# Optimization experiments

Measured on AMD Instinct MI355X. Metric: run time of the kernel, lower is better.

The kernel has to match this reference:

```python
import jax, jax.numpy as jnp
import numpy as np

B, L, D = 8, 3072, 256
E = 4            # num_experts
K = 2            # num_experts_per_tok
H = 4 * D        # expert mlp hidden
HS = 4 * D * 1   # shared expert hidden (n_shared_experts=1)


def setup_inputs() -> dict:
    key = jax.random.key(0)
    ks = jax.random.split(key, 16)
    s = lambda *sh: 1.0 / np.sqrt(sh[0])
    return {
        "context_c": jax.random.normal(ks[0], (B, L, D), jnp.float32),
        "time_cond": jax.random.normal(ks[1], (B, D), jnp.float32),
        "gate_w": jax.random.normal(ks[2], (3 * D, E), jnp.float32) * s(3 * D),
        "gate_b": jnp.zeros((E,), jnp.float32),
        "tmod_w": jax.random.normal(ks[3], (D, 2 * E), jnp.float32) * 0.02,
        "tmod_b": jnp.zeros((2 * E,), jnp.float32),
        "ew1": jax.random.normal(ks[4], (E, D, H), jnp.float32) * s(D),
        "eb1": jnp.zeros((E, H), jnp.float32),
        "ew2": jax.random.normal(ks[5], (E, H, D), jnp.float32) * s(H),
        "eb2": jnp.zeros((E, D), jnp.float32),
        "sw1": jax.random.normal(ks[6], (D, HS), jnp.float32) * s(D),
        "sb1": jnp.zeros((HS,), jnp.float32),
        "sw2": jax.random.normal(ks[7], (HS, D), jnp.float32) * s(HS),
        "sb2": jnp.zeros((D,), jnp.float32),
    }


def reference(context_c, time_cond, gate_w, gate_b, tmod_w, tmod_b,
              ew1, eb1, ew2, eb2, sw1, sb1, sw2, sb2):
    x = context_c
    Bc, Lc, Dc = x.shape
    Lh = Lw = Lc // 3
    Lp = Lc - Lh - Lw

    # modality aggregates for gating
    head, wrist, prop = x[:, :Lh], x[:, Lh:Lh + Lw], x[:, Lh + Lw:]
    full_agg = x.mean(axis=1)
    hp_agg = (head.sum(axis=1) + prop.sum(axis=1)) / (Lh + Lp)   # mean of cat(head, proprio)
    wp_agg = (wrist.sum(axis=1) + prop.sum(axis=1)) / (Lw + Lp)  # mean of cat(wrist, proprio)
    gate_in = jnp.concatenate([full_agg, hp_agg, wp_agg], axis=-1)  # (B, 3D)

    gate_logits = gate_in @ gate_w + gate_b  # (B, E)
    # time-conditioned modulation: SiLU -> Linear -> chunk(scale, shift)
    mod = jax.nn.silu(time_cond) @ tmod_w + tmod_b
    scale, shift = jnp.split(mod, 2, axis=-1)
    gate_logits = gate_logits * (1.0 + scale) + shift

    gate_scores = jax.nn.softmax(gate_logits, axis=-1)
    topk_w, topk_i = jax.lax.top_k(gate_scores, K)
    topk_w = topk_w / (topk_w.sum(axis=-1, keepdims=True) + 1e-8)

    # dense per-expert token-wise MLP (equivalent to the gather: MLPs act per-token)
    h = jax.nn.gelu(jnp.einsum('bld,edh->belh', x, ew1) + eb1[None, :, None, :], approximate=True)
    y = jnp.einsum('belh,ehd->beld', h, ew2) + eb2[None, :, None, :]  # (B, E, L, D)

    # modality masks: expert 0 & >=3 -> all tokens; 1 -> head+proprio; 2 -> wrist+proprio
    pos = jnp.arange(Lc)
    is_head = pos < Lh
    is_wrist = (pos >= Lh) & (pos < Lh + Lw)
    is_prop = pos >= Lh + Lw
    mask = jnp.ones((E, Lc), x.dtype)
    mask = mask.at[1].set((is_head | is_prop).astype(x.dtype))
    mask = mask.at[2].set((is_wrist | is_prop).astype(x.dtype))

    # combine weights per (batch, expert) from top-k
    w_be = (jax.nn.one_hot(topk_i, E, dtype=x.dtype) * topk_w[..., None]).sum(axis=1)  # (B, E)
    out = jnp.einsum('be,beld,el->bld', w_be, y, mask)

    # shared expert
    out = out + (jax.nn.gelu(x @ sw1 + sb1, approximate=True) @ sw2 + sb2)
    return out


if __name__ == '__main__':
    o = reference(**setup_inputs())
    print(o.shape, o.dtype)
```

## Files before the change

kernel.cpp:

```cpp
#include <hip/hip_runtime.h>
#include <stdint.h>

#define Ddim 256
#define Hdim 1024
#define LSEQ 3072

typedef __bf16 bf16x8 __attribute__((ext_vector_type(8)));
typedef unsigned short u16x8 __attribute__((ext_vector_type(8)));
typedef float f32x4 __attribute__((ext_vector_type(4)));

#define MFMA(a, b, c) __builtin_amdgcn_mfma_f32_16x16x32_bf16( \
    __builtin_bit_cast(bf16x8, (a)), __builtin_bit_cast(bf16x8, (b)), (c), 0, 0, 0)

__device__ __forceinline__ unsigned short f2bf(float f) {
  unsigned int u = __float_as_uint(f);
  u = u + 0x7FFFu + ((u >> 16) & 1u);
  return (unsigned short)(u >> 16);
}

__device__ __forceinline__ float gelu_t(float x) {
  float t = 0.7978845608028654f * (x + 0.044715f * x * x * x);
  float e = __expf(2.0f * t);
  float th = 1.0f - 2.0f / (e + 1.0f);
  return 0.5f * x * (1.0f + th);
}

__device__ __forceinline__ int gate_list(const float* __restrict__ wbe, int b, int seg,
                                         int* widx, float* wsc) {
  float wv0 = wbe[b * 4 + 0], wv1 = wbe[b * 4 + 1];
  float wv2 = wbe[b * 4 + 2], wv3 = wbe[b * 4 + 3];
  int nm = 0;
  widx[nm] = 4; wsc[nm] = 1.0f; ++nm;
  if (wv0 > 0.0f) { widx[nm] = 0; wsc[nm] = wv0; ++nm; }
  if (wv1 > 0.0f && seg != 1) { widx[nm] = 1; wsc[nm] = wv1; ++nm; }
  if (wv2 > 0.0f && seg != 0) { widx[nm] = 2; wsc[nm] = wv2; ++nm; }
  if (wv3 > 0.0f && nm < 3) { widx[nm] = 3; wsc[nm] = wv3; ++nm; }
  return nm;
}

__device__ __forceinline__ void glds16(const unsigned short* g, unsigned short* l) {
  __builtin_amdgcn_global_load_lds(
      (const __attribute__((address_space(1))) unsigned int*)g,
      (__attribute__((address_space(3))) unsigned int*)l, 16, 0, 0);
}


__global__ void zero_seg(float* p) {
  p[blockIdx.x * 256 + threadIdx.x] = 0.0f;
}

__global__ void seg_reduce(const float* __restrict__ x, float* __restrict__ seg) {
  int lb = blockIdx.x, b = blockIdx.y, tid = threadIdx.x;
  const float* xg = x + ((size_t)b * LSEQ + (size_t)lb * 128) * Ddim + tid;
  float s = 0.0f;
  #pragma unroll 8
  for (int r = 0; r < 128; ++r) s += xg[(size_t)r * Ddim];
  int sg = lb >> 3;
  atomicAdd(&seg[(b * 3 + sg) * Ddim + tid], s);
}

__global__ void gate_kernel(const float* __restrict__ seg, const float* __restrict__ tc,
                            const float* __restrict__ gw, const float* __restrict__ gb,
                            const float* __restrict__ tw, const float* __restrict__ tb,
                            float* __restrict__ wbe) {
  int b = threadIdx.x >> 6, lane = threadIdx.x & 63;
  const float* sb_ = seg + b * 3 * 256;
  float pl[4] = {0.f, 0.f, 0.f, 0.f};
  for (int i = lane; i < 768; i += 64) {
    int d = i & 255, rg = i >> 8;
    float Sh = sb_[d], Sw = sb_[256 + d], Sp = sb_[512 + d];
    float val = (rg == 0) ? (Sh + Sw + Sp) * (1.0f / 3072.0f)
              : (rg == 1) ? (Sh + Sp) * (1.0f / 2048.0f)
                          : (Sw + Sp) * (1.0f / 2048.0f);
    #pragma unroll
    for (int e = 0; e < 4; ++e) pl[e] += val * gw[i * 4 + e];
  }
  float pm[8] = {0.f, 0.f, 0.f, 0.f, 0.f, 0.f, 0.f, 0.f};
  for (int d = lane; d < 256; d += 64) {
    float t = tc[b * 256 + d];
    float s = t / (1.0f + __expf(-t));
    #pragma unroll
    for (int j = 0; j < 8; ++j) pm[j] += s * tw[d * 8 + j];
  }
  #pragma unroll
  for (int off = 32; off > 0; off >>= 1) {
    #pragma unroll
    for (int e = 0; e < 4; ++e) pl[e] += __shfl_down(pl[e], off);
    #pragma unroll
    for (int j = 0; j < 8; ++j) pm[j] += __shfl_down(pm[j], off);
  }
  if (lane == 0) {
    #pragma unroll
    for (int j = 0; j < 8; ++j) pm[j] += tb[j];
    float lg[4], sc[4];
    #pragma unroll
    for (int e = 0; e < 4; ++e) lg[e] = (pl[e] + gb[e]) * (1.0f + pm[e]) + pm[4 + e];
    float mx = fmaxf(fmaxf(lg[0], lg[1]), fmaxf(lg[2], lg[3]));
    float s = 0.0f;
    #pragma unroll
    for (int e = 0; e < 4; ++e) { sc[e] = __expf(lg[e] - mx); s += sc[e]; }
    #pragma unroll
    for (int e = 0; e < 4; ++e) sc[e] /= s;
    int i1 = 0;
    #pragma unroll
    for (int e = 1; e < 4; ++e) if (sc[e] > sc[i1]) i1 = e;
    int i2 = (i1 == 0) ? 1 : 0;
    #pragma unroll
    for (int e = 0; e < 4; ++e) if (e != i1 && sc[e] > sc[i2]) i2 = e;
    float den = sc[i1] + sc[i2] + 1e-8f;
    #pragma unroll
    for (int e = 0; e < 4; ++e)
      wbe[b * 4 + e] = (e == i1) ? sc[i1] / den : ((e == i2) ? sc[i2] / den : 0.0f);
  }
}


__global__ void prep_w1f_v2(const float* __restrict__ ew1, const float* __restrict__ sw1,
                            unsigned short* __restrict__ wch) {
  int hc = blockIdx.x, id = blockIdx.y;
  const float* src = (id < 4) ? (ew1 + (size_t)id * Ddim * Hdim) : sw1;
  __shared__ float tile[256 * 33];
  int tid = threadIdx.x;
  int h0 = hc * 32;
  #pragma unroll
  for (int p = 0; p < 8; ++p) {
    int row = p * 32 + (tid >> 3);
    int c = (tid & 7) * 4;
    float4 v = *(const float4*)&src[(size_t)row * Hdim + h0 + c];
    tile[row * 33 + c] = v.x; tile[row * 33 + c + 1] = v.y;
    tile[row * 33 + c + 2] = v.z; tile[row * 33 + c + 3] = v.w;
  }
  __syncthreads();
  unsigned short* dst = wch + ((size_t)(id * 32 + hc)) * 16384;
  int lane = tid & 63, lr = lane & 15, lg = lane >> 4;
  #pragma unroll
  for (int p = 0; p < 4; ++p) {
    int f = tid + p * 256;
    int hg = (f >> 6) & 1, k = f >> 7;
    u16x8 r;
    #pragma unroll
    for (int j = 0; j < 8; ++j) r[j] = f2bf(tile[(k * 32 + lg * 8 + j) * 33 + hg * 16 + lr]);
    *(u16x8*)&dst[(size_t)f * 8] = r;
  }
}

__global__ void prep_w2f_v2(const float* __restrict__ ew2, const float* __restrict__ sw2,
                            unsigned short* __restrict__ wch) {
  int hc = blockIdx.x, id = blockIdx.y;
  const float* src = (id < 4) ? (ew2 + (size_t)id * Hdim * Ddim) : sw2;
  __shared__ float tile[32 * 264];
  int tid = threadIdx.x;
  int h0 = hc * 32;
  #pragma unroll
  for (int p = 0; p < 8; ++p) {
    int hh = p * 4 + (tid >> 6);
    int c = (tid & 63) * 4;
    float4 v = *(const float4*)&src[(size_t)(h0 + hh) * Ddim + c];
    int ci = c + (c >> 5);
    tile[hh * 264 + ci] = v.x; tile[hh * 264 + ci + 1] = v.y;
    tile[hh * 264 + ci + 2] = v.z; tile[hh * 264 + ci + 3] = v.w;
  }
  __syncthreads();
  unsigned short* dst = wch + ((size_t)(id * 32 + hc)) * 16384 + 8192;
  int lane = tid & 63, lr = lane & 15, lg = lane >> 4;
  #pragma unroll
  for (int p = 0; p < 4; ++p) {
    int f = tid + p * 256;
    int dg = f >> 6;
    u16x8 r;
    #pragma unroll
    for (int j = 0; j < 8; ++j) {
      int c = dg * 16 + lr;
      r[j] = f2bf(tile[(lg * 8 + j) * 264 + c + (c >> 5)]);
    }
    *(u16x8*)&dst[(size_t)f * 8] = r;
  }
}

__global__ __launch_bounds__(256, 2) void moe_main(
    const float* __restrict__ x, const unsigned short* __restrict__ wch,
    const float* __restrict__ eb1, const float* __restrict__ sb1,
    const float* __restrict__ eb2, const float* __restrict__ sb2,
    const float* __restrict__ wbe, float* __restrict__ out) {
  __shared__ __align__(16) unsigned short lds[2 * 16384 + 64 * 40];
  unsigned short* hid = lds + 32768;

  const int i = blockIdx.x;
  const int b = i & 7, t = i >> 3;
  const int tid = threadIdx.x;
  const int wave = tid >> 6, lane = tid & 63;
  const int lr = lane & 15, lg = lane >> 4;
  const int wm = wave >> 1, wn = wave & 1;
  const int seg = t >> 4;

  int widx[3]; float wsc[3];
  const int nm = gate_list(wbe, b, seg, widx, wsc);
  const int total = nm * 32;

  u16x8 xf[8][2];
  const float* xb = x + ((size_t)(b * LSEQ + t * 64 + wm * 32 + lr)) * Ddim;
  #pragma unroll
  for (int k = 0; k < 8; ++k) {
    #pragma unroll
    for (int mf = 0; mf < 2; ++mf) {
      const float* p = xb + (size_t)(mf * 16) * Ddim + k * 32 + lg * 8;
      float4 v0 = *(const float4*)p;
      float4 v1 = *(const float4*)(p + 4);
      u16x8 r;
      r[0] = f2bf(v0.x); r[1] = f2bf(v0.y); r[2] = f2bf(v0.z); r[3] = f2bf(v0.w);
      r[4] = f2bf(v1.x); r[5] = f2bf(v1.y); r[6] = f2bf(v1.z); r[7] = f2bf(v1.w);
      xf[k][mf] = r;
    }
  }

  f32x4 oacc[4][4];
  const f32x4 fz = {0.f, 0.f, 0.f, 0.f};
  #pragma unroll
  for (int mf = 0; mf < 4; ++mf)
    #pragma unroll
    for (int nf = 0; nf < 4; ++nf) oacc[mf][nf] = fz;

  {
    const unsigned short* src = wch + (size_t)(widx[0] * 32) * 16384 + tid * 8;
    unsigned short* l = lds + tid * 8;
    #pragma unroll
    for (int q = 0; q < 8; ++q) glds16(src + q * 2048, l + q * 2048);
  }
  __syncthreads();

  for (int j = 0; j < total; ++j) {
    unsigned short* cur = lds + (j & 1) * 16384;
    unsigned short* nxt = lds + ((j & 1) ^ 1) * 16384;

    if (j + 1 < total) {
      int m2 = (j + 1) >> 5, hc2 = (j + 1) & 31;
      const unsigned short* src = wch + (size_t)(widx[m2] * 32 + hc2) * 16384 + tid * 8;
      unsigned short* l = nxt + tid * 8;
      #pragma unroll
      for (int q = 0; q < 8; ++q) glds16(src + q * 2048, l + q * 2048);
    }

    const int m = j >> 5, hc = j & 31;
    const float* b1g = (widx[m] < 4) ? (eb1 + widx[m] * Hdim) : sb1;
    const float wscale = wsc[m];

    f32x4 a1[2];
    a1[0] = fz; a1[1] = fz;
    #pragma unroll
    for (int k = 0; k < 8; ++k) {
      u16x8 bf = *(const u16x8*)&cur[((k * 2 + wn) * 64 + lane) * 8];
      a1[0] = MFMA(xf[k][0], bf, a1[0]);
      a1[1] = MFMA(xf[k][1], bf, a1[1]);
    }
    float b1v = b1g[hc * 32 + wn * 16 + lr];
    #pragma unroll
    for (int mr = 0; mr < 2; ++mr)
      #pragma unroll
      for (int r = 0; r < 4; ++r)
        hid[(wm * 32 + mr * 16 + lg * 4 + r) * 40 + wn * 16 + lr] =
            f2bf(gelu_t(a1[mr][r] + b1v) * wscale);
    __syncthreads();

    u16x8 ha[4], wb[4];
    #pragma unroll
    for (int mf = 0; mf < 4; ++mf)
      ha[mf] = *(const u16x8*)&hid[(mf * 16 + lr) * 40 + lg * 8];
    #pragma unroll
    for (int nf = 0; nf < 4; ++nf)
      wb[nf] = *(const u16x8*)&cur[8192 + ((wave * 4 + nf) * 64 + lane) * 8];
    #pragma unroll
    for (int mf = 0; mf < 4; ++mf)
      #pragma unroll
      for (int nf = 0; nf < 4; ++nf)
        oacc[mf][nf] = MFMA(ha[mf], wb[nf], oacc[mf][nf]);
    __syncthreads();
  }

  float* og = out + ((size_t)b * LSEQ + t * 64) * Ddim;
  #pragma unroll
  for (int nf = 0; nf < 4; ++nf) {
    int dcol = wave * 64 + nf * 16 + lr;
    float bias = sb2[dcol];
    for (int m = 0; m < nm; ++m)
      if (widx[m] < 4) bias += wsc[m] * eb2[widx[m] * Ddim + dcol];
    #pragma unroll
    for (int mf = 0; mf < 4; ++mf)
      #pragma unroll
      for (int r = 0; r < 4; ++r)
        og[(size_t)(mf * 16 + lg * 4 + r) * Ddim + dcol] = oacc[mf][nf][r] + bias;
  }
}


extern "C" void kernel_launch(void* const* d_in, const int* in_sizes, int n_in,
                              void* d_out, int out_size, void* d_ws, size_t ws_size,
                              hipStream_t stream) {
  const float* x      = (const float*)d_in[0];
  const float* tc     = (const float*)d_in[1];
  const float* gate_w = (const float*)d_in[2];
  const float* gate_b = (const float*)d_in[3];
  const float* tmod_w = (const float*)d_in[4];
  const float* tmod_b = (const float*)d_in[5];
  const float* ew1    = (const float*)d_in[6];
  const float* eb1    = (const float*)d_in[7];
  const float* ew2    = (const float*)d_in[8];
  const float* eb2    = (const float*)d_in[9];
  const float* sw1    = (const float*)d_in[10];
  const float* sb1    = (const float*)d_in[11];
  const float* sw2    = (const float*)d_in[12];
  const float* sb2    = (const float*)d_in[13];
  float* out = (float*)d_out;

  char* wsb = (char*)d_ws;
  float* ws_seg = (float*)wsb;
  float* ws_wbe = (float*)(wsb + 24576);
  unsigned short* wch = (unsigned short*)(wsb + 32768);

  zero_seg<<<24, 256, 0, stream>>>(ws_seg);
  seg_reduce<<<dim3(24, 8), 256, 0, stream>>>(x, ws_seg);
  gate_kernel<<<1, 512, 0, stream>>>(ws_seg, tc, gate_w, gate_b, tmod_w, tmod_b, ws_wbe);
  prep_w1f_v2<<<dim3(32, 5), 256, 0, stream>>>(ew1, sw1, wch);
  prep_w2f_v2<<<dim3(32, 5), 256, 0, stream>>>(ew2, sw2, wch);
  moe_main<<<384, 256, 0, stream>>>(x, wch, eb1, sb1, eb2, sb2, ws_wbe, out);
}
```

Measured before the change: 313.2 us.

## Split hidden dim across two blocks, fuse gating and prep kernels, triple-buffer weights

Merges the segment reduction and both weight-conversion kernels into one launch, and removes the atomics and zeroing by writing per-chunk partial sums. Gating now runs redundantly inside each main block. The hidden dimension is split in two halves across twice as many blocks, with a bf16 partial buffer and a combine kernel to add the halves. The main loop moves to a three-buffer async weight pipeline with explicit waitcnt, setprio and direct global loads of W2 fragments. This doubles grid parallelism and cuts launches, at the cost of an extra partial round-trip in bf16 and repeated gate work in every block.

```diff
diff --git a/kernel.cpp b/kernel.cpp
--- a/kernel.cpp
+++ b/kernel.cpp
@@ -25,155 +25,152 @@
   return 0.5f * x * (1.0f + th);
 }
 
-__device__ __forceinline__ int gate_list(const float* __restrict__ wbe, int b, int seg,
-                                         int* widx, float* wsc) {
-  float wv0 = wbe[b * 4 + 0], wv1 = wbe[b * 4 + 1];
-  float wv2 = wbe[b * 4 + 2], wv3 = wbe[b * 4 + 3];
-  int nm = 0;
-  widx[nm] = 4; wsc[nm] = 1.0f; ++nm;
-  if (wv0 > 0.0f) { widx[nm] = 0; wsc[nm] = wv0; ++nm; }
-  if (wv1 > 0.0f && seg != 1) { widx[nm] = 1; wsc[nm] = wv1; ++nm; }
-  if (wv2 > 0.0f && seg != 0) { widx[nm] = 2; wsc[nm] = wv2; ++nm; }
-  if (wv3 > 0.0f && nm < 3) { widx[nm] = 3; wsc[nm] = wv3; ++nm; }
-  return nm;
-}
-
 __device__ __forceinline__ void glds16(const unsigned short* g, unsigned short* l) {
   __builtin_amdgcn_global_load_lds(
       (const __attribute__((address_space(1))) unsigned int*)g,
       (__attribute__((address_space(3))) unsigned int*)l, 16, 0, 0);
 }
 
-
-__global__ void zero_seg(float* p) {
-  p[blockIdx.x * 256 + threadIdx.x] = 0.0f;
-}
-
-__global__ void seg_reduce(const float* __restrict__ x, float* __restrict__ seg) {
-  int lb = blockIdx.x, b = blockIdx.y, tid = threadIdx.x;
-  const float* xg = x + ((size_t)b * LSEQ + (size_t)lb * 128) * Ddim + tid;
-  float s = 0.0f;
-  #pragma unroll 8
-  for (int r = 0; r < 128; ++r) s += xg[(size_t)r * Ddim];
-  int sg = lb >> 3;
-  atomicAdd(&seg[(b * 3 + sg) * Ddim + tid], s);
-}
-
-__global__ void gate_kernel(const float* __restrict__ seg, const float* __restrict__ tc,
-                            const float* __restrict__ gw, const float* __restrict__ gb,
-                            const float* __restrict__ tw, const float* __restrict__ tb,
-                            float* __restrict__ wbe) {
-  int b = threadIdx.x >> 6, lane = threadIdx.x & 63;
-  const float* sb_ = seg + b * 3 * 256;
+__device__ __forceinline__ void gate_eval(
+    const float* __restrict__ part, const float* __restrict__ tc,
+    const float* __restrict__ gw, const float* __restrict__ gb,
+    const float* __restrict__ tw, const float* __restrict__ tb,
+    int b, int seg, int& nm, int& wi0, int& wi1, int& wi2,
+    float& sc0, float& sc1, float& sc2) {
+  int lane = threadIdx.x & 63;
   float pl[4] = {0.f, 0.f, 0.f, 0.f};
-  for (int i = lane; i < 768; i += 64) {
-    int d = i & 255, rg = i >> 8;
-    float Sh = sb_[d], Sw = sb_[256 + d], Sp = sb_[512 + d];
-    float val = (rg == 0) ? (Sh + Sw + Sp) * (1.0f / 3072.0f)
-              : (rg == 1) ? (Sh + Sp) * (1.0f / 2048.0f)
-                          : (Sw + Sp) * (1.0f / 2048.0f);
-    #pragma unroll
-    for (int e = 0; e < 4; ++e) pl[e] += val * gw[i * 4 + e];
-  }
   float pm[8] = {0.f, 0.f, 0.f, 0.f, 0.f, 0.f, 0.f, 0.f};
   for (int d = lane; d < 256; d += 64) {
+    float Sh = 0.f, Sw = 0.f, Sp = 0.f;
+    #pragma unroll
+    for (int lb = 0; lb < 8; ++lb)  Sh += part[(size_t)(b * 24 + lb) * 256 + d];
+    #pragma unroll
+    for (int lb = 8; lb < 16; ++lb) Sw += part[(size_t)(b * 24 + lb) * 256 + d];
+    #pragma unroll
+    for (int lb = 16; lb < 24; ++lb) Sp += part[(size_t)(b * 24 + lb) * 256 + d];
+    float vF = (Sh + Sw + Sp) * (1.0f / 3072.0f);
+    float vH = (Sh + Sp) * (1.0f / 2048.0f);
+    float vW = (Sw + Sp) * (1.0f / 2048.0f);
+    #pragma unroll
+    for (int e = 0; e < 4; ++e)
+      pl[e] += vF * gw[d * 4 + e] + vH * gw[(256 + d) * 4 + e] + vW * gw[(512 + d) * 4 + e];
     float t = tc[b * 256 + d];
     float s = t / (1.0f + __expf(-t));
     #pragma unroll
     for (int j = 0; j < 8; ++j) pm[j] += s * tw[d * 8 + j];
   }
   #pragma unroll
-  for (int off = 32; off > 0; off >>= 1) {
-    #pragma unroll
-    for (int e = 0; e < 4; ++e) pl[e] += __shfl_down(pl[e], off);
-    #pragma unroll
-    for (int j = 0; j < 8; ++j) pm[j] += __shfl_down(pm[j], off);
-  }
-  if (lane == 0) {
-    #pragma unroll
-    for (int j = 0; j < 8; ++j) pm[j] += tb[j];
-    float lg[4], sc[4];
-    #pragma unroll
-    for (int e = 0; e < 4; ++e) lg[e] = (pl[e] + gb[e]) * (1.0f + pm[e]) + pm[4 + e];
-    float mx = fmaxf(fmaxf(lg[0], lg[1]), fmaxf(lg[2], lg[3]));
+  for (int off = 1; off < 64; off <<= 1) {
+    #pragma unroll
+    for (int e = 0; e < 4; ++e) pl[e] += __shfl_xor(pl[e], off);
+    #pragma unroll
+    for (int j = 0; j < 8; ++j) pm[j] += __shfl_xor(pm[j], off);
+  }
+  #pragma unroll
+  for (int j = 0; j < 8; ++j) pm[j] += tb[j];
+  float lg[4], sc[4];
+  #pragma unroll
+  for (int e = 0; e < 4; ++e) lg[e] = (pl[e] + gb[e]) * (1.0f + pm[e]) + pm[4 + e];
+  float mx = fmaxf(fmaxf(lg[0], lg[1]), fmaxf(lg[2], lg[3]));
+  float s = 0.0f;
+  #pragma unroll
+  for (int e = 0; e < 4; ++e) { sc[e] = __expf(lg[e] - mx); s += sc[e]; }
+  #pragma unroll
+  for (int e = 0; e < 4; ++e) sc[e] /= s;
+  int i1 = 0;
+  #pragma unroll
+  for (int e = 1; e < 4; ++e) if (sc[e] > sc[i1]) i1 = e;
+  int i2 = (i1 == 0) ? 1 : 0;
+  #pragma unroll
+  for (int e = 0; e < 4; ++e) if (e != i1 && sc[e] > sc[i2]) i2 = e;
+  float den = sc[i1] + sc[i2] + 1e-8f;
+  float w0 = 0.f, w1 = 0.f, w2v = 0.f, w3 = 0.f;
+  #pragma unroll
+  for (int e = 0; e < 4; ++e) {
+    float v = (e == i1) ? sc[i1] / den : ((e == i2) ? sc[i2] / den : 0.0f);
+    if (e == 0) w0 = v; else if (e == 1) w1 = v; else if (e == 2) w2v = v; else w3 = v;
+  }
+  nm = 0;
+  int widx[3]; float wsc[3];
+  widx[nm] = 4; wsc[nm] = 1.0f; ++nm;
+  if (w0 > 0.0f) { widx[nm] = 0; wsc[nm] = w0; ++nm; }
+  if (w1 > 0.0f && seg != 1) { widx[nm] = 1; wsc[nm] = w1; ++nm; }
+  if (w2v > 0.0f && seg != 0) { widx[nm] = 2; wsc[nm] = w2v; ++nm; }
+  if (w3 > 0.0f && nm < 3) { widx[nm] = 3; wsc[nm] = w3; ++nm; }
+  wi0 = widx[0];
+  wi1 = (nm > 1) ? widx[1] : widx[0];
+  wi2 = (nm > 2) ? widx[2] : wi1;
+  sc0 = wsc[0];
+  sc1 = (nm > 1) ? wsc[1] : 0.f;
+  sc2 = (nm > 2) ? wsc[2] : 0.f;
+}
+
+__global__ void k1_prep(const float* __restrict__ x, float* __restrict__ part,
+                        const float* __restrict__ ew1, const float* __restrict__ sw1,
+                        const float* __restrict__ ew2, const float* __restrict__ sw2,
+                        unsigned short* __restrict__ wch) {
+  __shared__ float tile[8448];
+  int i = blockIdx.x, tid = threadIdx.x;
+  if (i < 192) {
+    int lb = i % 24, b = i / 24;
+    const float* xg = x + ((size_t)b * LSEQ + (size_t)lb * 128) * Ddim + tid;
     float s = 0.0f;
-    #pragma unroll
-    for (int e = 0; e < 4; ++e) { sc[e] = __expf(lg[e] - mx); s += sc[e]; }
-    #pragma unroll
-    for (int e = 0; e < 4; ++e) sc[e] /= s;
-    int i1 = 0;
-    #pragma unroll
-    for (int e = 1; e < 4; ++e) if (sc[e] > sc[i1]) i1 = e;
-    int i2 = (i1 == 0) ? 1 : 0;
-    #pragma unroll
-    for (int e = 0; e < 4; ++e) if (e != i1 && sc[e] > sc[i2]) i2 = e;
-    float den = sc[i1] + sc[i2] + 1e-8f;
-    #pragma unroll
-    for (int e = 0; e < 4; ++e)
-      wbe[b * 4 + e] = (e == i1) ? sc[i1] / den : ((e == i2) ? sc[i2] / den : 0.0f);
-  }
-}
-
-
-__global__ void prep_w1f_v2(const float* __restrict__ ew1, const float* __restrict__ sw1,
-                            unsigned short* __restrict__ wch) {
-  int hc = blockIdx.x, id = blockIdx.y;
-  const float* src = (id < 4) ? (ew1 + (size_t)id * Ddim * Hdim) : sw1;
-  __shared__ float tile[256 * 33];
-  int tid = threadIdx.x;
+    #pragma unroll 8
+    for (int r = 0; r < 128; ++r) s += xg[(size_t)r * Ddim];
+    part[(size_t)(b * 24 + lb) * 256 + tid] = s;
+    return;
+  }
+  int pid = i - 192;
+  int z = pid / 160, rem = pid % 160;
+  int id = rem / 32, hc = rem % 32;
+  int lane = tid & 63, lr = lane & 15, lg = lane >> 4;
   int h0 = hc * 32;
-  #pragma unroll
-  for (int p = 0; p < 8; ++p) {
-    int row = p * 32 + (tid >> 3);
-    int c = (tid & 7) * 4;
-    float4 v = *(const float4*)&src[(size_t)row * Hdim + h0 + c];
-    tile[row * 33 + c] = v.x; tile[row * 33 + c + 1] = v.y;
-    tile[row * 33 + c + 2] = v.z; tile[row * 33 + c + 3] = v.w;
-  }
-  __syncthreads();
-  unsigned short* dst = wch + ((size_t)(id * 32 + hc)) * 16384;
-  int lane = tid & 63, lr = lane & 15, lg = lane >> 4;
-  #pragma unroll
-  for (int p = 0; p < 4; ++p) {
-    int f = tid + p * 256;
-    int hg = (f >> 6) & 1, k = f >> 7;
-    u16x8 r;
-    #pragma unroll
-    for (int j = 0; j < 8; ++j) r[j] = f2bf(tile[(k * 32 + lg * 8 + j) * 33 + hg * 16 + lr]);
-    *(u16x8*)&dst[(size_t)f * 8] = r;
-  }
-}
-
-__global__ void prep_w2f_v2(const float* __restrict__ ew2, const float* __restrict__ sw2,
-                            unsigned short* __restrict__ wch) {
-  int hc = blockIdx.x, id = blockIdx.y;
-  const float* src = (id < 4) ? (ew2 + (size_t)id * Hdim * Ddim) : sw2;
-  __shared__ float tile[32 * 264];
-  int tid = threadIdx.x;
-  int h0 = hc * 32;
-  #pragma unroll
-  for (int p = 0; p < 8; ++p) {
-    int hh = p * 4 + (tid >> 6);
-    int c = (tid & 63) * 4;
-    float4 v = *(const float4*)&src[(size_t)(h0 + hh) * Ddim + c];
-    int ci = c + (c >> 5);
-    tile[hh * 264 + ci] = v.x; tile[hh * 264 + ci + 1] = v.y;
-    tile[hh * 264 + ci + 2] = v.z; tile[hh * 264 + ci + 3] = v.w;
-  }
-  __syncthreads();
-  unsigned short* dst = wch + ((size_t)(id * 32 + hc)) * 16384 + 8192;
-  int lane = tid & 63, lr = lane & 15, lg = lane >> 4;
-  #pragma unroll
-  for (int p = 0; p < 4; ++p) {
-    int f = tid + p * 256;
-    int dg = f >> 6;
-    u16x8 r;
-    #pragma unroll
-    for (int j = 0; j < 8; ++j) {
-      int c = dg * 16 + lr;
-      r[j] = f2bf(tile[(lg * 8 + j) * 264 + c + (c >> 5)]);
-    }
-    *(u16x8*)&dst[(size_t)f * 8] = r;
+  if (z == 0) {
+    const float* src = (id < 4) ? (ew1 + (size_t)id * Ddim * Hdim) : sw1;
+    #pragma unroll
+    for (int p = 0; p < 8; ++p) {
+      int row = p * 32 + (tid >> 3);
+      int c = (tid & 7) * 4;
+      float4 v = *(const float4*)&src[(size_t)row * Hdim + h0 + c];
+      tile[row * 33 + c] = v.x; tile[row * 33 + c + 1] = v.y;
+      tile[row * 33 + c + 2] = v.z; tile[row * 33 + c + 3] = v.w;
+    }
+    __syncthreads();
+    unsigned short* dst = wch + ((size_t)(id * 32 + hc)) * 16384;
+    #pragma unroll
+    for (int p = 0; p < 4; ++p) {
+      int f = tid + p * 256;
+      int hg = (f >> 6) & 1, k = f >> 7;
+      u16x8 r;
+      #pragma unroll
+      for (int j = 0; j < 8; ++j) r[j] = f2bf(tile[(k * 32 + lg * 8 + j) * 33 + hg * 16 + lr]);
+      *(u16x8*)&dst[(size_t)f * 8] = r;
+    }
+  } else {
+    const float* src = (id < 4) ? (ew2 + (size_t)id * Hdim * Ddim) : sw2;
+    #pragma unroll
+    for (int p = 0; p < 8; ++p) {
+      int hh = p * 4 + (tid >> 6);
+      int c = (tid & 63) * 4;
+      float4 v = *(const float4*)&src[(size_t)(h0 + hh) * Ddim + c];
+      int ci = c + (c >> 5);
+      tile[hh * 264 + ci] = v.x; tile[hh * 264 + ci + 1] = v.y;
+      tile[hh * 264 + ci + 2] = v.z; tile[hh * 264 + ci + 3] = v.w;
+    }
+    __syncthreads();
+    unsigned short* dst = wch + ((size_t)(id * 32 + hc)) * 16384 + 8192;
+    #pragma unroll
+    for (int p = 0; p < 4; ++p) {
+      int f = tid + p * 256;
+      int dg = f >> 6;
+      u16x8 r;
+      #pragma unroll
+      for (int j = 0; j < 8; ++j) {
+        int c = dg * 16 + lr;
+        r[j] = f2bf(tile[(lg * 8 + j) * 264 + c + (c >> 5)]);
+      }
+      *(u16x8*)&dst[(size_t)f * 8] = r;
+    }
   }
 }
 
@@ -181,21 +178,25 @@
     const float* __restrict__ x, const unsigned short* __restrict__ wch,
     const float* __restrict__ eb1, const float* __restrict__ sb1,
     const float* __restrict__ eb2, const float* __restrict__ sb2,
-    const float* __restrict__ wbe, float* __restrict__ out) {
-  __shared__ __align__(16) unsigned short lds[2 * 16384 + 64 * 40];
-  unsigned short* hid = lds + 32768;
+    const float* __restrict__ part, const float* __restrict__ tc,
+    const float* __restrict__ gw, const float* __restrict__ gb,
+    const float* __restrict__ tw, const float* __restrict__ tb,
+    unsigned short* __restrict__ kpart, float* __restrict__ out) {
+  __shared__ __align__(16) unsigned short lds[3 * 8192 + 64 * 40];
+  unsigned short* const hid = lds + 3 * 8192;
 
   const int i = blockIdx.x;
-  const int b = i & 7, t = i >> 3;
+  const int b = i & 7, q = (i >> 3) & 1, t = i >> 4;
   const int tid = threadIdx.x;
   const int wave = tid >> 6, lane = tid & 63;
   const int lr = lane & 15, lg = lane >> 4;
   const int wm = wave >> 1, wn = wave & 1;
   const int seg = t >> 4;
 
-  int widx[3]; float wsc[3];
-  const int nm = gate_list(wbe, b, seg, widx, wsc);
-  const int total = nm * 32;
+  int nm, wi0, wi1, wi2;
+  float sc0, sc1, sc2;
+  gate_eval(part, tc, gw, gb, tw, tb, b, seg, nm, wi0, wi1, wi2, sc0, sc1, sc2);
+  const int total = nm * 16;
 
   u16x8 xf[8][2];
   const float* xb = x + ((size_t)(b * LSEQ + t * 64 + wm * 32 + lr)) * Ddim;
@@ -220,75 +221,133 @@
     #pragma unroll
     for (int nf = 0; nf < 4; ++nf) oacc[mf][nf] = fz;
 
+  unsigned short* p0 = lds;
+  unsigned short* p1 = lds + 8192;
+  unsigned short* p2 = lds + 16384;
+
   {
-    const unsigned short* src = wch + (size_t)(widx[0] * 32) * 16384 + tid * 8;
-    unsigned short* l = lds + tid * 8;
-    #pragma unroll
-    for (int q = 0; q < 8; ++q) glds16(src + q * 2048, l + q * 2048);
-  }
-  __syncthreads();
+    const unsigned short* c0 = wch + (size_t)(wi0 * 32 + q * 16) * 16384;
+    #pragma unroll
+    for (int qq = 0; qq < 4; ++qq) glds16(c0 + tid * 8 + qq * 2048, p0 + tid * 8 + qq * 2048);
+    int j1 = (total > 1) ? 1 : 0;
+    int id1 = (j1 >> 4) == 0 ? wi0 : wi1;
+    const unsigned short* c1 = wch + (size_t)(id1 * 32 + q * 16 + (j1 & 15)) * 16384;
+    #pragma unroll
+    for (int qq = 0; qq < 4; ++qq) glds16(c1 + tid * 8 + qq * 2048, p1 + tid * 8 + qq * 2048);
+  }
+  asm volatile("s_waitcnt vmcnt(4)" ::: "memory");
+  __builtin_amdgcn_s_barrier();
+  __builtin_amdgcn_sched_barrier(0);
 
   for (int j = 0; j < total; ++j) {
-    unsigned short* cur = lds + (j & 1) * 16384;
-    unsigned short* nxt = lds + ((j & 1) ^ 1) * 16384;
-
-    if (j + 1 < total) {
-      int m2 = (j + 1) >> 5, hc2 = (j + 1) & 31;
-      const unsigned short* src = wch + (size_t)(widx[m2] * 32 + hc2) * 16384 + tid * 8;
-      unsigned short* l = nxt + tid * 8;
-      #pragma unroll
-      for (int q = 0; q < 8; ++q) glds16(src + q * 2048, l + q * 2048);
-    }
-
-    const int m = j >> 5, hc = j & 31;
-    const float* b1g = (widx[m] < 4) ? (eb1 + widx[m] * Hdim) : sb1;
-    const float wscale = wsc[m];
+    const int m = j >> 4, hc = q * 16 + (j & 15);
+    const int id = (m == 0) ? wi0 : ((m == 1) ? wi1 : wi2);
+    const float wscale = (m == 0) ? sc0 : ((m == 1) ? sc1 : sc2);
+    const unsigned short* cb = wch + (size_t)(id * 32 + hc) * 16384;
+
+    const float* b1g = (id < 4) ? (eb1 + id * Hdim) : sb1;
+    float b1v = b1g[hc * 32 + wn * 16 + lr];
+    u16x8 wbU[4];
+    const unsigned short* w2c = cb + 8192 + ((size_t)(wave * 4) * 64 + lane) * 8;
+    #pragma unroll
+    for (int nf = 0; nf < 4; ++nf) wbU[nf] = *(const u16x8*)(w2c + nf * 512);
+    __builtin_amdgcn_sched_barrier(0);
+
+    {
+      int j2 = (j + 2 < total) ? j + 2 : total - 1;
+      int m2 = j2 >> 4;
+      int id2 = (m2 == 0) ? wi0 : ((m2 == 1) ? wi1 : wi2);
+      const unsigned short* cb2 = wch + (size_t)(id2 * 32 + q * 16 + (j2 & 15)) * 16384;
+      #pragma unroll
+      for (int qq = 0; qq < 4; ++qq)
+        glds16(cb2 + tid * 8 + qq * 2048, p2 + tid * 8 + qq * 2048);
+    }
+    __builtin_amdgcn_sched_barrier(0);
+
+    asm volatile("s_waitcnt vmcnt(18)" ::: "memory");
+    __builtin_amdgcn_sched_barrier(0);
 
     f32x4 a1[2];
     a1[0] = fz; a1[1] = fz;
+    __builtin_amdgcn_s_setprio(1);
     #pragma unroll
     for (int k = 0; k < 8; ++k) {
-      u16x8 bf = *(const u16x8*)&cur[((k * 2 + wn) * 64 + lane) * 8];
+      u16x8 bf = *(const u16x8*)&p0[((k * 2 + wn) * 64 + lane) * 8];
       a1[0] = MFMA(xf[k][0], bf, a1[0]);
       a1[1] = MFMA(xf[k][1], bf, a1[1]);
     }
-    float b1v = b1g[hc * 32 + wn * 16 + lr];
+    __builtin_amdgcn_s_setprio(0);
     #pragma unroll
     for (int mr = 0; mr < 2; ++mr)
       #pragma unroll
       for (int r = 0; r < 4; ++r)
         hid[(wm * 32 + mr * 16 + lg * 4 + r) * 40 + wn * 16 + lr] =
             f2bf(gelu_t(a1[mr][r] + b1v) * wscale);
-    __syncthreads();
-
-    u16x8 ha[4], wb[4];
+    asm volatile("s_waitcnt lgkmcnt(0)" ::: "memory");
+    __builtin_amdgcn_s_barrier();
+    __builtin_amdgcn_sched_barrier(0);
+
+    u16x8 ha[4];
     #pragma unroll
     for (int mf = 0; mf < 4; ++mf)
       ha[mf] = *(const u16x8*)&hid[(mf * 16 + lr) * 40 + lg * 8];
-    #pragma unroll
-    for (int nf = 0; nf < 4; ++nf)
-      wb[nf] = *(const u16x8*)&cur[8192 + ((wave * 4 + nf) * 64 + lane) * 8];
+    __builtin_amdgcn_s_setprio(1);
     #pragma unroll
     for (int mf = 0; mf < 4; ++mf)
       #pragma unroll
       for (int nf = 0; nf < 4; ++nf)
-        oacc[mf][nf] = MFMA(ha[mf], wb[nf], oacc[mf][nf]);
-    __syncthreads();
-  }
-
-  float* og = out + ((size_t)b * LSEQ + t * 64) * Ddim;
-  #pragma unroll
-  for (int nf = 0; nf < 4; ++nf) {
-    int dcol = wave * 64 + nf * 16 + lr;
-    float bias = sb2[dcol];
-    for (int m = 0; m < nm; ++m)
-      if (widx[m] < 4) bias += wsc[m] * eb2[widx[m] * Ddim + dcol];
-    #pragma unroll
-    for (int mf = 0; mf < 4; ++mf)
-      #pragma unroll
-      for (int r = 0; r < 4; ++r)
-        og[(size_t)(mf * 16 + lg * 4 + r) * Ddim + dcol] = oacc[mf][nf][r] + bias;
-  }
+        oacc[mf][nf] = MFMA(ha[mf], wbU[nf], oacc[mf][nf]);
+    __builtin_amdgcn_s_setprio(0);
+    __builtin_amdgcn_s_barrier();
+    __builtin_amdgcn_sched_barrier(0);
+
+    unsigned short* tmp = p0; p0 = p1; p1 = p2; p2 = tmp;
+  }
+
+  if (q == 0) {
+    float* og = out + ((size_t)b * LSEQ + t * 64) * Ddim;
+    #pragma unroll
+    for (int nf = 0; nf < 4; ++nf) {
+      int dcol = wave * 64 + nf * 16 + lr;
+      float bias = sb2[dcol];
+      if (wi0 < 4) bias += sc0 * eb2[wi0 * Ddim + dcol];
+      if (nm > 1 && wi1 < 4) bias += sc1 * eb2[wi1 * Ddim + dcol];
+      if (nm > 2 && wi2 < 4) bias += sc2 * eb2[wi2 * Ddim + dcol];
+      #pragma unroll
+      for (int mf = 0; mf < 4; ++mf)
+        #pragma unroll
+        for (int r = 0; r < 4; ++r)
+          og[(size_t)(mf * 16 + lg * 4 + r) * Ddim + dcol] = oacc[mf][nf][r] + bias;
+    }
+  } else {
+    unsigned short* pg = kpart + ((size_t)b * LSEQ + t * 64) * Ddim;
+    #pragma unroll
+    for (int nf = 0; nf < 4; ++nf) {
+      int dcol = wave * 64 + nf * 16 + lr;
+      #pragma unroll
+      for (int mf = 0; mf < 4; ++mf)
+        #pragma unroll
+        for (int r = 0; r < 4; ++r)
+          pg[(size_t)(mf * 16 + lg * 4 + r) * Ddim + dcol] = f2bf(oacc[mf][nf][r]);
+    }
+  }
+}
+
+__global__ void combine(const unsigned short* __restrict__ kpart, float* __restrict__ out) {
+  size_t base = ((size_t)blockIdx.x * 256 + threadIdx.x) * 8;
+  u16x8 p = *(const u16x8*)&kpart[base];
+  float4 o0 = *(const float4*)&out[base];
+  float4 o1 = *(const float4*)&out[base + 4];
+  o0.x += __uint_as_float((unsigned)p[0] << 16);
+  o0.y += __uint_as_float((unsigned)p[1] << 16);
+  o0.z += __uint_as_float((unsigned)p[2] << 16);
+  o0.w += __uint_as_float((unsigned)p[3] << 16);
+  o1.x += __uint_as_float((unsigned)p[4] << 16);
+  o1.y += __uint_as_float((unsigned)p[5] << 16);
+  o1.z += __uint_as_float((unsigned)p[6] << 16);
+  o1.w += __uint_as_float((unsigned)p[7] << 16);
+  *(float4*)&out[base] = o0;
+  *(float4*)&out[base + 4] = o1;
 }
 
 
@@ -312,14 +371,12 @@
   float* out = (float*)d_out;
 
   char* wsb = (char*)d_ws;
-  float* ws_seg = (float*)wsb;
-  float* ws_wbe = (float*)(wsb + 24576);
-  unsigned short* wch = (unsigned short*)(wsb + 32768);
-
-  zero_seg<<<24, 256, 0, stream>>>(ws_seg);
-  seg_reduce<<<dim3(24, 8), 256, 0, stream>>>(x, ws_seg);
-  gate_kernel<<<1, 512, 0, stream>>>(ws_seg, tc, gate_w, gate_b, tmod_w, tmod_b, ws_wbe);
-  prep_w1f_v2<<<dim3(32, 5), 256, 0, stream>>>(ew1, sw1, wch);
-  prep_w2f_v2<<<dim3(32, 5), 256, 0, stream>>>(ew2, sw2, wch);
-  moe_main<<<384, 256, 0, stream>>>(x, wch, eb1, sb1, eb2, sb2, ws_wbe, out);
-}
+  float* ws_part = (float*)wsb;
+  unsigned short* wch = (unsigned short*)(wsb + 196608);
+  unsigned short* kpart = (unsigned short*)(wsb + 196608 + 10485760);
+
+  k1_prep<<<512, 256, 0, stream>>>(x, ws_part, ew1, sw1, ew2, sw2, wch);
+  moe_main<<<768, 256, 0, stream>>>(x, wch, eb1, sb1, eb2, sb2, ws_part, tc,
+                                    gate_w, gate_b, tmod_w, tmod_b, kpart, out);
+  combine<<<3072, 256, 0, stream>>>(kpart, out);
+}
```

Result: faster. 270.2 us (-13.7%).
